# Performance work log

Hardware: AMD Instinct MI355X
Metric: run time of the kernel (lower is better)

## Reference

```python
import jax, jax.numpy as jnp
import numpy as np

B, T, H = 8, 512, 1024
NA, NP = 1024, 512
NW, WD = 16, 20          # num_width_embeddings, span_width_embedding_dim
NCLS = 66
K_ARG, K_PRED = 30, 15   # constant_arg / constant_pred caps
NEG = -1e20


def _gather_seq(seq, idx):
    # seq [B,T,D], idx [B,...] int -> [B,...,D]
    b = seq.shape[0]
    flat = idx.reshape(b, -1)
    out = jnp.take_along_axis(seq, flat[..., None], axis=1)
    return out.reshape(idx.shape + (seq.shape[-1],))


def _endpoint(features, spans, mask, W_width=None):
    mi = mask.astype(spans.dtype)
    starts = spans[..., 0] * mi
    ends = spans[..., 1] * mi
    parts = [_gather_seq(features, starts), _gather_seq(features, ends)]
    if W_width is not None:
        widths = jnp.clip(ends - starts, 0, NW - 1)
        parts.append(W_width[widths])
    return jnp.concatenate(parts, -1) * mask[..., None]


def _attentive(features, spans, mask, W_att, b_att):
    # global attention logits over all tokens [B,T]
    logits = (features @ W_att + b_att)[..., 0]
    starts, ends = spans[..., 0], spans[..., 1]
    widths = ends - starts                              # [B,N]
    r = jnp.arange(NW)                                  # static max span width
    span_mask = (r[None, None, :] <= widths[..., None])
    raw = ends[..., None] - r[None, None, :]            # AllenNLP indexes end backwards
    span_mask = span_mask & (raw >= 0)
    idx = jnp.maximum(raw, 0)                           # [B,N,W]
    emb = _gather_seq(features, idx)                    # [B,N,W,H]
    att = _gather_seq(logits[..., None], idx)[..., 0]   # [B,N,W]
    att = jnp.where(span_mask, att, -1e30)
    w = jax.nn.softmax(att, axis=-1) * span_mask
    attended = jnp.einsum('bnw,bnwh->bnh', w, emb)
    return attended * mask[..., None]


def _prune(emb, mask, num_keep, K, W1, b1, W2, b2):
    h = jax.nn.relu(emb @ W1 + b1)
    scores = h @ W2 + b2                                # [B,N,1]
    scores = jnp.where(mask[..., None] > 0, scores, NEG)
    _, top_idx = jax.lax.top_k(scores[..., 0], K)       # [B,K]
    keep = jnp.arange(K)[None, :] < num_keep[:, None]
    fill = jnp.max(top_idx, axis=1, keepdims=True)
    top_idx = jnp.where(keep, top_idx, fill)
    top_idx = jnp.sort(top_idx, axis=1)
    top_emb = jnp.take_along_axis(emb, top_idx[..., None], axis=1)
    seq_mask = jnp.take_along_axis(mask, top_idx, axis=1) > 0
    top_mask = (keep & seq_mask).astype(jnp.float32)
    top_scores = jnp.take_along_axis(scores, top_idx[..., None], axis=1)
    return top_emb, top_mask, top_idx, top_scores, scores


def setup_inputs() -> dict:
    key = jax.random.key(0)
    ks = jax.random.split(key, 16)
    features = jax.random.normal(ks[0], (B, T, H), jnp.float32)
    a_start = jax.random.randint(ks[1], (B, NA), 1, T - NW)
    a_width = jax.random.randint(ks[2], (B, NA), 0, NW)
    arg_candidates = jnp.stack([a_start, a_start + a_width], -1)
    p_start = jax.random.randint(ks[3], (B, NP), 1, T - 3)
    p_width = jax.random.randint(ks[4], (B, NP), 0, 3)
    predicate_candidates = jnp.stack([p_start, p_start + p_width], -1)

    def lin(k, i, o):
        return jax.random.normal(k, (i, o), jnp.float32) / np.sqrt(i)

    arg_dim = 3 * H + WD
    pred_dim = 2 * H
    return dict(
        features=features,
        arg_candidates=arg_candidates,
        predicate_candidates=predicate_candidates,
        W_width=jax.random.normal(ks[5], (NW, WD), jnp.float32) * 0.02,
        W_att=lin(ks[6], H, 1), b_att=jnp.zeros((1,), jnp.float32),
        Wa1=lin(ks[7], arg_dim, H), ba1=jnp.zeros((H,), jnp.float32),
        Wa2=lin(ks[8], H, 1), ba2=jnp.zeros((1,), jnp.float32),
        Wp1=lin(ks[9], pred_dim, H), bp1=jnp.zeros((H,), jnp.float32),
        Wp2=lin(ks[10], H, 1), bp2=jnp.zeros((1,), jnp.float32),
        Ws1=lin(ks[11], arg_dim + pred_dim, H), bs1=jnp.zeros((H,), jnp.float32),
        Ws2=lin(ks[12], H, NCLS - 1), bs2=jnp.zeros((NCLS - 1,), jnp.float32),
    )


def reference(features, arg_candidates, predicate_candidates, W_width, W_att, b_att,
              Wa1, ba1, Wa2, ba2, Wp1, bp1, Wp2, bp2, Ws1, bs1, Ws2, bs2):
    arg_mask = (arg_candidates[..., 1] > 0).astype(jnp.float32)
    pred_mask = (predicate_candidates[..., 1] > 0).astype(jnp.float32)

    # KENTON_LEE arg repr: endpoint (start,end,width-emb) + self-attentive
    ep = _endpoint(features, arg_candidates, arg_mask, W_width)
    at = _attentive(features, arg_candidates, arg_mask, W_att, b_att)
    arg_emb = jnp.concatenate([ep, at], -1)             # [B,NA,3H+WD]

    n_keep_arg = jnp.minimum((arg_mask.sum(-1) * 0.8).astype(jnp.int32), K_ARG)
    (top_arg_emb, top_arg_mask, top_arg_idx,
     top_arg_scores, arg_full_scores) = _prune(arg_emb, arg_mask, n_keep_arg, K_ARG, Wa1, ba1, Wa2, ba2)

    # KENTON_LEE pred repr: endpoints only (2H)
    pred_emb = _endpoint(features, predicate_candidates, pred_mask, None)
    n_keep_pred = jnp.minimum((pred_mask.sum(-1) * 0.4).astype(jnp.int32), K_PRED)
    (top_pred_emb, top_pred_mask, top_pred_idx,
     top_pred_scores, pred_full_scores) = _prune(pred_emb, pred_mask, n_keep_pred, K_PRED, Wp1, bp1, Wp2, bp2)

    top_arg_spans = jnp.take_along_axis(arg_candidates, top_arg_idx[..., None], axis=1)
    top_pred_spans = jnp.take_along_axis(predicate_candidates, top_pred_idx[..., None], axis=1)

    # pairwise scorer: concat([pred, arg]) @ Ws1 == pred@Ws1[:Dp] + arg@Ws1[Dp:]
    dp = top_pred_emb.shape[-1]
    pred_proj = top_pred_emb @ Ws1[:dp]                 # [B,Kp,H]
    arg_proj = top_arg_emb @ Ws1[dp:]                   # [B,Ka,H]
    h = jax.nn.relu(pred_proj[:, :, None, :] + arg_proj[:, None, :, :] + bs1)
    scores = h @ Ws2 + bs2                              # [B,Kp,Ka,NCLS-1]
    scores = scores + top_arg_scores[:, None, :, :] + top_pred_scores[:, :, None, :]
    dummy = jnp.zeros(scores.shape[:-1] + (1,), scores.dtype)
    srl_scores = jnp.concatenate([dummy, scores], -1)   # [B,Kp,Ka,NCLS]

    return (srl_scores, top_pred_spans, top_arg_spans, top_pred_mask,
            top_arg_mask, pred_full_scores, arg_full_scores)
```

## Files before the change

### kernel.cpp

```cpp
#include <hip/hip_runtime.h>
#include <math.h>

#define BB 8
#define TT 512
#define HH 1024
#define NAc 1024
#define NPc 512
#define NWc 16
#define WDc 20
#define NCLSc 66
#define KARG 30
#define KPRED 15
#define NEGV (-1e20f)

typedef __bf16 bf16x8 __attribute__((ext_vector_type(8)));
typedef float  f32x4  __attribute__((ext_vector_type(4)));

#define OFF_PAS   0
#define OFF_PAE   (OFF_PAS  + BB*TT*HH)
#define OFF_PATT  (OFF_PAE  + BB*TT*HH)
#define OFF_PPS   (OFF_PATT + BB*TT*HH)
#define OFF_PPE   (OFF_PPS  + BB*TT*HH)
#define OFF_END_A (OFF_PPE  + BB*TT*HH)
#define OFF_AEMB  OFF_PAS
#define OFF_PEMB  OFF_PAE
#define OFF_CPA   OFF_PATT
#define OFF_CPP   OFF_PPS
#define OFF_APROJ OFF_PPE
#define OFF_PPROJ (OFF_PPE + BB*KARG*HH)
#define OFF_LOG   OFF_END_A
#define OFF_WT    (OFF_LOG  + BB*TT)
#define OFF_AIDX  (OFF_WT   + NWc*HH)
#define OFF_PIDX  (OFF_AIDX + BB*KARG)
#define OFF_ASC   (OFF_PIDX + BB*KPRED)
#define OFF_PSC   (OFF_ASC  + BB*KARG)
#define OFF_SPLIT (OFF_PSC + BB*KPRED)
#define XSLAB_U   (4096*1024)
#define WSLAB_U   (5*1024*1024)

#define O_SRL 0
#define O_TPS (O_SRL + BB*KPRED*KARG*NCLSc)
#define O_TAS (O_TPS + BB*KPRED*2)
#define O_TPM (O_TAS + BB*KARG*2)
#define O_TAM (O_TPM + BB*KPRED)
#define O_PFS (O_TAM + BB*KARG)
#define O_AFS (O_PFS + BB*NPc)

__device__ inline float4 f4_add(const float4&a,const float4&b){return make_float4(a.x+b.x,a.y+b.y,a.z+b.z,a.w+b.w);}
__device__ inline float4 f4_fma(float c,const float4&v,const float4&a){return make_float4(fmaf(c,v.x,a.x),fmaf(c,v.y,a.y),fmaf(c,v.z,a.z),fmaf(c,v.w,a.w));}
__device__ inline float4 f4_scale(const float4&v,float c){return make_float4(v.x*c,v.y*c,v.z*c,v.w*c);}
__device__ inline float4 f4_relu(const float4&v){return make_float4(fmaxf(v.x,0.f),fmaxf(v.y,0.f),fmaxf(v.z,0.f),fmaxf(v.w,0.f));}

__device__ inline unsigned short bf16r(float f) {
  unsigned int u = __float_as_uint(f);
  u = (u + 0x7FFFu + ((u >> 16) & 1u)) >> 16;
  return (unsigned short)u;
}
__device__ inline float bf2f(unsigned short h) { return __uint_as_float(((unsigned int)h) << 16); }

__device__ inline f32x4 mfma16(bf16x8 a, bf16x8 b, f32x4 c) {
  return __builtin_amdgcn_mfma_f32_16x16x32_bf16(a, b, c, 0, 0, 0);
}

__global__ __launch_bounds__(256) void k_logits(const float* __restrict__ f, const float* __restrict__ Watt,
    const float* __restrict__ batt, float* __restrict__ lg) {
  const int lane = threadIdx.x & 63, wv = threadIdx.x >> 6;
  const int r = blockIdx.x*4 + wv;
  const float4* x = (const float4*)&f[(size_t)r*HH];
  const float4* wt = (const float4*)Watt;
  float s = 0.f;
  #pragma unroll
  for (int i=0;i<4;++i) {
    const float4 v = x[lane + i*64];
    const float4 w = wt[lane + i*64];
    s += v.x*w.x + v.y*w.y + v.z*w.z + v.w*w.w;
  }
  for (int o=32;o>0;o>>=1) s += __shfl_down(s,o,64);
  if (lane==0) lg[r] = s + batt[0];
}

__global__ __launch_bounds__(256) void k_wtab(const float* __restrict__ Wwidth, const float* __restrict__ src,
    float* __restrict__ WT) {
  const int w = blockIdx.x; const int j = threadIdx.x*4;
  float4 acc = make_float4(0,0,0,0);
  for (int d=0; d<WDc; ++d) {
    const float c = Wwidth[w*WDc+d];
    const float4 v = *(const float4*)&src[d*HH + j];
    acc = f4_fma(c, v, acc);
  }
  *(float4*)&WT[w*HH + j] = acc;
}

__global__ __launch_bounds__(256) void k_splitX(const float* __restrict__ f,
    unsigned short* __restrict__ X0, unsigned short* __restrict__ X1, unsigned short* __restrict__ X2) {
  const size_t i = ((size_t)blockIdx.x*256 + threadIdx.x) * 4;
  const float4 v = *(const float4*)&f[i];
  ushort4 h0, h1, h2;
  float a[4] = {v.x, v.y, v.z, v.w};
  unsigned short r0[4], r1[4], r2[4];
  #pragma unroll
  for (int q=0;q<4;++q) {
    r0[q] = bf16r(a[q]);            float rem1 = a[q] - bf2f(r0[q]);
    r1[q] = bf16r(rem1);            float rem2 = rem1 - bf2f(r1[q]);
    r2[q] = bf16r(rem2);
  }
  h0 = make_ushort4(r0[0],r0[1],r0[2],r0[3]);
  h1 = make_ushort4(r1[0],r1[1],r1[2],r1[3]);
  h2 = make_ushort4(r2[0],r2[1],r2[2],r2[3]);
  *(ushort4*)&X0[i] = h0;
  *(ushort4*)&X1[i] = h1;
  *(ushort4*)&X2[i] = h2;
}

__global__ __launch_bounds__(256) void k_splitW(const float* __restrict__ Wa1, const float* __restrict__ Wp1,
    unsigned short* __restrict__ W0, unsigned short* __restrict__ W1, unsigned short* __restrict__ W2) {
  const int part = blockIdx.z;
  const float* srcs[5] = {Wa1, Wa1 + 1024*1024, Wa1 + 2068*1024, Wp1, Wp1 + 1024*1024};
  const float* __restrict__ src = srcs[part];
  const size_t po = (size_t)part * 1024 * 1024;
  const int k0 = blockIdx.x * 32, n0 = blockIdx.y * 32;
  __shared__ float tile[32][33];
  const int c = threadIdx.x & 31, r0 = threadIdx.x >> 5;
  #pragma unroll
  for (int q=0;q<4;++q) {
    const int row = r0 + 8*q;
    tile[row][c] = src[(size_t)(k0+row)*1024 + n0 + c];
  }
  __syncthreads();
  #pragma unroll
  for (int q=0;q<4;++q) {
    const int nl = r0 + 8*q;
    const float v = tile[c][nl];
    const unsigned short h0 = bf16r(v);   const float rem1 = v - bf2f(h0);
    const unsigned short h1 = bf16r(rem1); const float rem2 = rem1 - bf2f(h1);
    const unsigned short h2 = bf16r(rem2);
    const size_t oi = po + (size_t)(n0+nl)*1024 + k0 + c;
    W0[oi] = h0; W1[oi] = h1; W2[oi] = h2;
  }
}

__global__ __launch_bounds__(256) void k_mgemm(
    const unsigned short* __restrict__ X0, const unsigned short* __restrict__ X1, const unsigned short* __restrict__ X2,
    const unsigned short* __restrict__ W0, const unsigned short* __restrict__ W1, const unsigned short* __restrict__ W2,
    float* __restrict__ proj) {
  const int part = blockIdx.z;
  const int rb = blockIdx.x * 128, cb = blockIdx.y * 128;
  float* __restrict__ C = proj + (size_t)part * (4096*1024);
  const size_t po = (size_t)part * 1024 * 1024;
  const unsigned short* Xs[3] = {X0, X1, X2};
  const unsigned short* Bs_[3] = {W0 + po, W1 + po, W2 + po};

  __shared__ unsigned short As[3][128*40];
  __shared__ unsigned short Bs[3][128*40];

  const int tid = threadIdx.x;
  const int lane = tid & 63, wave = tid >> 6;
  const int wr = wave >> 1, wc = wave & 1;
  const int r16 = lane & 15, g8 = (lane >> 4) * 8;

  f32x4 acc[4][4];
  #pragma unroll
  for (int i=0;i<4;++i)
    #pragma unroll
    for (int j=0;j<4;++j) acc[i][j] = (f32x4){0.f,0.f,0.f,0.f};

  for (int k0 = 0; k0 < 1024; k0 += 32) {
    for (int i = tid; i < 1536; i += 256) {
      const int slab = i >> 9, rem = i & 511, seg = rem & 3, row = rem >> 2;
      const unsigned short* src = Xs[slab] + (size_t)(rb + row) * 1024 + k0 + seg * 8;
      *(uint4*)&As[slab][row*40 + seg*8] = *(const uint4*)src;
    }
    for (int i = tid; i < 1536; i += 256) {
      const int slab = i >> 9, rem = i & 511, seg = rem & 3, row = rem >> 2;
      const unsigned short* src = Bs_[slab] + (size_t)(cb + row) * 1024 + k0 + seg * 8;
      *(uint4*)&Bs[slab][row*40 + seg*8] = *(const uint4*)src;
    }
    __syncthreads();

    bf16x8 a[3][4];
    #pragma unroll
    for (int mf=0; mf<4; ++mf) {
      const int rowi = (wr*64 + mf*16 + r16) * 40 + g8;
      a[0][mf] = *reinterpret_cast<const bf16x8*>(&As[0][rowi]);
      a[1][mf] = *reinterpret_cast<const bf16x8*>(&As[1][rowi]);
      a[2][mf] = *reinterpret_cast<const bf16x8*>(&As[2][rowi]);
    }
    #pragma unroll
    for (int nf=0; nf<4; ++nf) {
      const int rowi = (wc*64 + nf*16 + r16) * 40 + g8;
      const bf16x8 b0 = *reinterpret_cast<const bf16x8*>(&Bs[0][rowi]);
      const bf16x8 b1 = *reinterpret_cast<const bf16x8*>(&Bs[1][rowi]);
      const bf16x8 b2 = *reinterpret_cast<const bf16x8*>(&Bs[2][rowi]);
      #pragma unroll
      for (int mf=0; mf<4; ++mf) {
        f32x4 t = acc[mf][nf];
        t = mfma16(a[0][mf], b0, t);
        t = mfma16(a[0][mf], b1, t);
        t = mfma16(a[1][mf], b0, t);
        t = mfma16(a[1][mf], b1, t);
        t = mfma16(a[0][mf], b2, t);
        t = mfma16(a[2][mf], b0, t);
        acc[mf][nf] = t;
      }
    }
    __syncthreads();
  }

  const int colb = cb + wc*64 + r16;
  const int rowb = rb + wr*64 + (lane >> 4) * 4;
  #pragma unroll
  for (int mf=0; mf<4; ++mf)
    #pragma unroll
    for (int nf=0; nf<4; ++nf)
      #pragma unroll
      for (int r=0; r<4; ++r)
        C[(size_t)(rowb + mf*16 + r) * 1024 + colb + nf*16] = acc[mf][nf][r];
}

__device__ inline void att_weights(const float* __restrict__ logits, int b, int sr, int er,
                                   float aw[16], int idxs[16]) {
  const int wdt = er - sr;
  float mx = -1e30f;
  #pragma unroll
  for (int w=0; w<16; ++w) {
    const bool valid = (w <= wdt) && (er - w >= 0);
    idxs[w] = max(er - w, 0);
    aw[w] = valid ? logits[b*TT + idxs[w]] : -1e30f;
    mx = fmaxf(mx, aw[w]);
  }
  float ssum = 0.f;
  #pragma unroll
  for (int w=0; w<16; ++w) { aw[w] = expf(aw[w]-mx); ssum += aw[w]; }
  const float inv = 1.f/ssum;
  #pragma unroll
  for (int w=0; w<16; ++w) {
    const bool valid = (w <= wdt) && (er - w >= 0);
    aw[w] = valid ? aw[w]*inv : 0.f;
  }
}

__global__ __launch_bounds__(256) void k_argscore(const int* __restrict__ cand,
    const float* __restrict__ logits, const float* __restrict__ Pas, const float* __restrict__ Pae,
    const float* __restrict__ Patt, const float* __restrict__ WT,
    const float* __restrict__ ba1, const float* __restrict__ Wa2, const float* __restrict__ ba2,
    float* __restrict__ osc) {
  const int g = blockIdx.x;
  const int b = g >> 10;
  const int t = threadIdx.x;
  const int sr = cand[g*2], er = cand[g*2+1];
  if (er <= 0) { if (t==0) osc[g] = NEGV; return; }
  const int s = sr, e = er;
  const int wc = min(max(e - s, 0), NWc-1);
  float aw[16]; int idxs[16];
  att_weights(logits, b, sr, er, aw, idxs);
  float4 h = ((const float4*)&Pas[(size_t)(b*TT+s)*HH])[t];
  h = f4_add(h, ((const float4*)&Pae[(size_t)(b*TT+e)*HH])[t]);
  h = f4_add(h, ((const float4*)&WT[(size_t)wc*HH])[t]);
  #pragma unroll
  for (int w=0; w<16; ++w) if (aw[w] != 0.f) {
    const float4 v = ((const float4*)&Patt[(size_t)(b*TT+idxs[w])*HH])[t];
    h = f4_fma(aw[w], v, h);
  }
  h = f4_add(h, ((const float4*)ba1)[t]);
  h = f4_relu(h);
  const float4 w2 = ((const float4*)Wa2)[t];
  float part = h.x*w2.x + h.y*w2.y + h.z*w2.z + h.w*w2.w;
  for (int o=32;o>0;o>>=1) part += __shfl_down(part,o,64);
  __shared__ float red[4];
  const int lane = t & 63, wvi = t >> 6;
  if (lane==0) red[wvi] = part;
  __syncthreads();
  if (t==0) osc[g] = red[0]+red[1]+red[2]+red[3] + ba2[0];
}

__global__ __launch_bounds__(256) void k_predscore(const int* __restrict__ cand,
    const float* __restrict__ Pps, const float* __restrict__ Ppe,
    const float* __restrict__ bp1, const float* __restrict__ Wp2, const float* __restrict__ bp2,
    float* __restrict__ osc) {
  const int g = blockIdx.x;
  const int b = g >> 9;
  const int t = threadIdx.x;
  const int sr = cand[g*2], er = cand[g*2+1];
  if (er <= 0) { if (t==0) osc[g] = NEGV; return; }
  float4 h = ((const float4*)&Pps[(size_t)(b*TT+sr)*HH])[t];
  h = f4_add(h, ((const float4*)&Ppe[(size_t)(b*TT+er)*HH])[t]);
  h = f4_add(h, ((const float4*)bp1)[t]);
  h = f4_relu(h);
  const float4 w2 = ((const float4*)Wp2)[t];
  float part = h.x*w2.x + h.y*w2.y + h.z*w2.z + h.w*w2.w;
  for (int o=32;o>0;o>>=1) part += __shfl_down(part,o,64);
  __shared__ float red[4];
  const int lane = t & 63, wvi = t >> 6;
  if (lane==0) red[wvi] = part;
  __syncthreads();
  if (t==0) osc[g] = red[0]+red[1]+red[2]+red[3] + bp2[0];
}

__global__ __launch_bounds__(256) void k_topk(const float* __restrict__ fullsc, const int* __restrict__ cand,
    int N, int K, float frac, float* __restrict__ o_spans, float* __restrict__ o_mask,
    float* __restrict__ o_tsc, int* __restrict__ o_idx) {
  const int b = blockIdx.x;
  const int t = threadIdx.x;
  __shared__ float sv[1024];
  __shared__ int sel[32];
  __shared__ float bv[4]; __shared__ int bi[4];
  __shared__ int mcnt; __shared__ int snk;
  const float* sc = fullsc + (size_t)b*N;
  const int* cd = cand + (size_t)b*N*2;
  if (t==0) mcnt = 0;
  __syncthreads();
  int cnt = 0;
  for (int i=t;i<N;i+=256){ sv[i]=sc[i]; if (cd[i*2+1] > 0) cnt++; }
  atomicAdd(&mcnt, cnt);
  __syncthreads();
  const int lane = t & 63, wvi = t >> 6;
  for (int k=0;k<K;++k) {
    float best = -INFINITY; int bidx = 1<<30;
    for (int i=t;i<N;i+=256){ const float v=sv[i]; if (v>best){best=v;bidx=i;} }
    for (int o=32;o>0;o>>=1){
      const float v2 = __shfl_down(best,o,64); const int i2 = __shfl_down(bidx,o,64);
      if (v2>best || (v2==best && i2<bidx)) {best=v2;bidx=i2;}
    }
    if (lane==0){bv[wvi]=best;bi[wvi]=bidx;}
    __syncthreads();
    if (t==0){
      float bb=bv[0]; int ii=bi[0];
      for (int w=1;w<4;++w){ if (bv[w]>bb || (bv[w]==bb && bi[w]<ii)){bb=bv[w];ii=bi[w];} }
      sel[k]=ii; sv[ii] = -INFINITY;
    }
    __syncthreads();
  }
  if (t==0) {
    int nk = (int)((float)mcnt * frac); if (nk > K) nk = K;
    snk = nk;
    int fill = 0;
    for (int k=0;k<K;++k) fill = max(fill, sel[k]);
    for (int k=nk;k<K;++k) sel[k] = fill;
    for (int k=1;k<K;++k){ int v=sel[k]; int j=k-1; while(j>=0 && sel[j]>v){sel[j+1]=sel[j];--j;} sel[j+1]=v; }
  }
  __syncthreads();
  if (t < K) {
    const int id = sel[t];
    const int s0 = cd[id*2], e0 = cd[id*2+1];
    o_spans[(b*K+t)*2]   = (float)s0;
    o_spans[(b*K+t)*2+1] = (float)e0;
    o_mask[b*K+t] = (t < snk && e0 > 0) ? 1.f : 0.f;
    o_tsc[b*K+t] = sc[id];
    o_idx[b*K+t] = id;
  }
}

__global__ __launch_bounds__(256) void k_build_pemb(const float* __restrict__ f, const int* __restrict__ cand,
    const int* __restrict__ tidx, float* __restrict__ Pemb) {
  const int r = blockIdx.x;
  const int b = r / KPRED;
  const int id = tidx[r];
  int s = cand[(b*NPc+id)*2], e = cand[(b*NPc+id)*2+1];
  const float mf = (e > 0) ? 1.f : 0.f;
  if (e <= 0) { s = 0; e = 0; }
  const int t = threadIdx.x;
  const float4 fs = ((const float4*)&f[(size_t)(b*TT+s)*HH])[t];
  const float4 fe = ((const float4*)&f[(size_t)(b*TT+e)*HH])[t];
  float4* o = (float4*)&Pemb[(size_t)r*2048];
  o[t]     = f4_scale(fs, mf);
  o[256+t] = f4_scale(fe, mf);
}

__global__ __launch_bounds__(256) void k_build_aemb(const float* __restrict__ f, const int* __restrict__ cand,
    const int* __restrict__ tidx, const float* __restrict__ logits, const float* __restrict__ Wwidth,
    float* __restrict__ Aemb) {
  const int r = blockIdx.x;
  const int b = r / KARG;
  const int id = tidx[r];
  const int sr = cand[(b*NAc+id)*2], er = cand[(b*NAc+id)*2+1];
  const float mf = (er > 0) ? 1.f : 0.f;
  const int s = (er > 0) ? sr : 0, e = (er > 0) ? er : 0;
  const int wc = min(max(e - s, 0), NWc-1);
  float aw[16]; int idxs[16];
  att_weights(logits, b, sr, er, aw, idxs);
  const int t = threadIdx.x;
  float* rowp = &Aemb[(size_t)r*3092];
  const float4 fs  = ((const float4*)&f[(size_t)(b*TT+s)*HH])[t];
  const float4 fe4 = ((const float4*)&f[(size_t)(b*TT+e)*HH])[t];
  ((float4*)rowp)[t]        = f4_scale(fs, mf);
  ((float4*)(rowp+1024))[t] = f4_scale(fe4, mf);
  if (t < WDc) rowp[2048+t] = Wwidth[wc*WDc+t]*mf;
  float4 acc = make_float4(0,0,0,0);
  #pragma unroll
  for (int w=0; w<16; ++w) if (aw[w] != 0.f) {
    const float4 fv = ((const float4*)&f[(size_t)(b*TT+idxs[w])*HH])[t];
    acc = f4_fma(aw[w], fv, acc);
  }
  ((float4*)(rowp+2068))[t] = f4_scale(acc, mf);
}

template<int MT>
__global__ __launch_bounds__(256) void k_sgemm(const float* __restrict__ A, int lda, int K,
                                               const float* __restrict__ W, float* __restrict__ Cp) {
  const int ct = blockIdx.x;
  const int b  = blockIdx.y;
  const int kz = blockIdx.z;
  const int Mtotal = 8*MT;
  const int cbase = ct*128;
  const int rbase = b*MT;
  const int klen = K/4;
  const int kbeg = kz*klen, kend = kbeg + klen;
  __shared__ float As[MT][64];
  const int tid = threadIdx.x;
  const int lane = tid & 63, wv = tid >> 6;
  const int ks = lane & 7;
  const int cg = wv*8 + (lane >> 3);
  const int col = cbase + cg*4;
  float acc[MT][4];
  #pragma unroll
  for (int m=0;m<MT;++m){acc[m][0]=0.f;acc[m][1]=0.f;acc[m][2]=0.f;acc[m][3]=0.f;}
  for (int k0 = kbeg; k0 < kend; k0 += 64) {
    const int kc = min(64, kend - k0);
    for (int i = tid; i < MT*64; i += 256) {
      const int m = i >> 6, kk = i & 63;
      As[m][kk] = (kk < kc) ? A[(size_t)(rbase+m)*lda + k0 + kk] : 0.f;
    }
    __syncthreads();
    const int kmax = min(8, kc - ks*8);
    for (int i = 0; i < kmax; ++i) {
      const int kk = ks*8 + i;
      const float4 wv4 = *(const float4*)&W[(size_t)(k0+kk)*1024 + col];
      #pragma unroll
      for (int m=0;m<MT;++m) {
        const float av = As[m][kk];
        acc[m][0] = fmaf(av, wv4.x, acc[m][0]);
        acc[m][1] = fmaf(av, wv4.y, acc[m][1]);
        acc[m][2] = fmaf(av, wv4.z, acc[m][2]);
        acc[m][3] = fmaf(av, wv4.w, acc[m][3]);
      }
    }
    __syncthreads();
  }
  #pragma unroll
  for (int m=0;m<MT;++m) {
    #pragma unroll
    for (int j=0;j<4;++j) {
      float v = acc[m][j];
      v += __shfl_xor(v, 1, 64);
      v += __shfl_xor(v, 2, 64);
      v += __shfl_xor(v, 4, 64);
      acc[m][j] = v;
    }
  }
  if (ks == 0) {
    #pragma unroll
    for (int m=0;m<MT;++m) {
      const float4 v = make_float4(acc[m][0],acc[m][1],acc[m][2],acc[m][3]);
      *(float4*)&Cp[((size_t)kz*Mtotal + rbase + m)*1024 + col] = v;
    }
  }
}

__global__ void k_reduce4(const float* __restrict__ Cp, float* __restrict__ Co, int n) {
  const int i = blockIdx.x*256 + threadIdx.x;
  if (i < n) Co[i] = Cp[i] + Cp[(size_t)n+i] + Cp[2*(size_t)n+i] + Cp[3*(size_t)n+i];
}

__global__ __launch_bounds__(256) void k_final(const float* __restrict__ pproj, const float* __restrict__ aproj,
    const float* __restrict__ bs1, const float* __restrict__ Ws2, const float* __restrict__ bs2,
    const float* __restrict__ tasc, const float* __restrict__ tpsc, float* __restrict__ srl) {
  const int g = blockIdx.x;
  const int b = g / (KPRED*KARG);
  const int rem = g % (KPRED*KARG);
  const int p = rem / KARG, a = rem % KARG;
  const int t = threadIdx.x;
  __shared__ float h[1024];
  __shared__ float part[4][64];
  __shared__ float r64[4];
  {
    const float4 pv = ((const float4*)&pproj[(size_t)(b*KPRED+p)*HH])[t];
    const float4 av = ((const float4*)&aproj[(size_t)(b*KARG+a)*HH])[t];
    const float4 bv = ((const float4*)bs1)[t];
    float4 v;
    v.x = fmaxf(pv.x+av.x+bv.x, 0.f);
    v.y = fmaxf(pv.y+av.y+bv.y, 0.f);
    v.z = fmaxf(pv.z+av.z+bv.z, 0.f);
    v.w = fmaxf(pv.w+av.w+bv.w, 0.f);
    ((float4*)h)[t] = v;
  }
  __syncthreads();
  const int j = t & 63, sl = t >> 6;
  float accj = 0.f, acc64 = 0.f;
  const int kb = sl*256;
  for (int kk = kb; kk < kb+256; ++kk) {
    const float hv = h[kk];
    accj = fmaf(hv, Ws2[(size_t)kk*65 + j], accj);
    if (j == 0) acc64 = fmaf(hv, Ws2[(size_t)kk*65 + 64], acc64);
  }
  part[sl][j] = accj;
  if (j == 0) r64[sl] = acc64;
  __syncthreads();
  const float base = tasc[b*KARG+a] + tpsc[b*KPRED+p];
  float* o = &srl[(size_t)g*NCLSc];
  if (t < 64) {
    o[1+t] = part[0][t]+part[1][t]+part[2][t]+part[3][t] + bs2[t] + base;
  } else if (t == 64) {
    o[0] = 0.f;
    o[65] = r64[0]+r64[1]+r64[2]+r64[3] + bs2[64] + base;
  }
}

extern "C" void kernel_launch(void* const* d_in, const int* in_sizes, int n_in,
                              void* d_out, int out_size, void* d_ws, size_t ws_size,
                              hipStream_t stream) {
  const float* features = (const float*)d_in[0];
  const int*   argc_    = (const int*)d_in[1];
  const int*   predc    = (const int*)d_in[2];
  const float* Wwidth   = (const float*)d_in[3];
  const float* Watt     = (const float*)d_in[4];
  const float* batt     = (const float*)d_in[5];
  const float* Wa1      = (const float*)d_in[6];
  const float* ba1      = (const float*)d_in[7];
  const float* Wa2      = (const float*)d_in[8];
  const float* ba2      = (const float*)d_in[9];
  const float* Wp1      = (const float*)d_in[10];
  const float* bp1      = (const float*)d_in[11];
  const float* Wp2      = (const float*)d_in[12];
  const float* bp2      = (const float*)d_in[13];
  const float* Ws1      = (const float*)d_in[14];
  const float* bs1      = (const float*)d_in[15];
  const float* Ws2      = (const float*)d_in[16];
  const float* bs2      = (const float*)d_in[17];
  float* ws  = (float*)d_ws;
  float* out = (float*)d_out;

  unsigned short* X0 = (unsigned short*)(ws + OFF_SPLIT);
  unsigned short* X1 = X0 + XSLAB_U;
  unsigned short* X2 = X1 + XSLAB_U;
  unsigned short* W0 = X2 + XSLAB_U;
  unsigned short* W1 = W0 + WSLAB_U;
  unsigned short* W2 = W1 + WSLAB_U;

  k_logits<<<dim3(BB*TT/4), 256, 0, stream>>>(features, Watt, batt, ws + OFF_LOG);
  k_wtab<<<dim3(NWc), 256, 0, stream>>>(Wwidth, Wa1 + 2048*1024, ws + OFF_WT);
  k_splitX<<<dim3(4096), 256, 0, stream>>>(features, X0, X1, X2);
  k_splitW<<<dim3(32, 32, 5), 256, 0, stream>>>(Wa1, Wp1, W0, W1, W2);
  k_mgemm<<<dim3(32, 8, 5), 256, 0, stream>>>(X0, X1, X2, W0, W1, W2, ws + OFF_PAS);
  k_argscore<<<dim3(BB*NAc), 256, 0, stream>>>(argc_, ws + OFF_LOG, ws + OFF_PAS, ws + OFF_PAE,
      ws + OFF_PATT, ws + OFF_WT, ba1, Wa2, ba2, out + O_AFS);
  k_predscore<<<dim3(BB*NPc), 256, 0, stream>>>(predc, ws + OFF_PPS, ws + OFF_PPE,
      bp1, Wp2, bp2, out + O_PFS);
  k_topk<<<dim3(BB), 256, 0, stream>>>(out + O_AFS, argc_, NAc, KARG, 0.8f,
      out + O_TAS, out + O_TAM, ws + OFF_ASC, (int*)(ws + OFF_AIDX));
  k_topk<<<dim3(BB), 256, 0, stream>>>(out + O_PFS, predc, NPc, KPRED, 0.4f,
      out + O_TPS, out + O_TPM, ws + OFF_PSC, (int*)(ws + OFF_PIDX));
  k_build_aemb<<<dim3(BB*KARG), 256, 0, stream>>>(features, argc_, (const int*)(ws + OFF_AIDX),
      ws + OFF_LOG, Wwidth, ws + OFF_AEMB);
  k_build_pemb<<<dim3(BB*KPRED), 256, 0, stream>>>(features, predc, (const int*)(ws + OFF_PIDX),
      ws + OFF_PEMB);
  k_sgemm<KARG><<<dim3(8, 8, 4), 256, 0, stream>>>(ws + OFF_AEMB, 3092, 3092, Ws1 + (size_t)2048*1024, ws + OFF_CPA);
  k_sgemm<KPRED><<<dim3(8, 8, 4), 256, 0, stream>>>(ws + OFF_PEMB, 2048, 2048, Ws1, ws + OFF_CPP);
  k_reduce4<<<dim3((BB*KARG*HH + 255)/256), 256, 0, stream>>>(ws + OFF_CPA, ws + OFF_APROJ, BB*KARG*HH);
  k_reduce4<<<dim3((BB*KPRED*HH + 255)/256), 256, 0, stream>>>(ws + OFF_CPP, ws + OFF_PPROJ, BB*KPRED*HH);
  k_final<<<dim3(BB*KPRED*KARG), 256, 0, stream>>>(ws + OFF_PPROJ, ws + OFF_APROJ,
      bs1, Ws2, bs2, ws + OFF_ASC, ws + OFF_PSC, out + O_SRL);
}
```

Baseline: 955.2 us.

## Restructure split-bf16 GEMM into six passes with direct global-to-LDS loads

The three-way split-bf16 GEMM no longer stages all three slabs of A and B in shared memory per k-step. It now runs six sequential passes over the term pairs (X0W0, X0W1, X1W0, X1W1, X0W2, X2W0), each loading a 128x64 tile straight into LDS with global_load_lds. This cuts LDS footprint and register pressure and removes the VGPR round-trip on loads, which may raise occupancy. The cost is that each A/B slab is re-read from global memory several times, and the unpadded 64-wide LDS rows may cause bank conflicts on the fragment reads.

```diff
diff --git a/kernel.cpp b/kernel.cpp
--- a/kernel.cpp
+++ b/kernel.cpp
@@ -15,6 +15,9 @@
 
 typedef __bf16 bf16x8 __attribute__((ext_vector_type(8)));
 typedef float  f32x4  __attribute__((ext_vector_type(4)));
+
+#define LDS_U32(p) ((__attribute__((address_space(3))) unsigned int*)(p))
+#define GLB_U32(p) ((const __attribute__((address_space(1))) unsigned int*)(p))
 
 #define OFF_PAS   0
 #define OFF_PAE   (OFF_PAS  + BB*TT*HH)
@@ -95,7 +98,6 @@
     unsigned short* __restrict__ X0, unsigned short* __restrict__ X1, unsigned short* __restrict__ X2) {
   const size_t i = ((size_t)blockIdx.x*256 + threadIdx.x) * 4;
   const float4 v = *(const float4*)&f[i];
-  ushort4 h0, h1, h2;
   float a[4] = {v.x, v.y, v.z, v.w};
   unsigned short r0[4], r1[4], r2[4];
   #pragma unroll
@@ -104,12 +106,9 @@
     r1[q] = bf16r(rem1);            float rem2 = rem1 - bf2f(r1[q]);
     r2[q] = bf16r(rem2);
   }
-  h0 = make_ushort4(r0[0],r0[1],r0[2],r0[3]);
-  h1 = make_ushort4(r1[0],r1[1],r1[2],r1[3]);
-  h2 = make_ushort4(r2[0],r2[1],r2[2],r2[3]);
-  *(ushort4*)&X0[i] = h0;
-  *(ushort4*)&X1[i] = h1;
-  *(ushort4*)&X2[i] = h2;
+  *(ushort4*)&X0[i] = make_ushort4(r0[0],r0[1],r0[2],r0[3]);
+  *(ushort4*)&X1[i] = make_ushort4(r1[0],r1[1],r1[2],r1[3]);
+  *(ushort4*)&X2[i] = make_ushort4(r2[0],r2[1],r2[2],r2[3]);
 }
 
 __global__ __launch_bounds__(256) void k_splitW(const float* __restrict__ Wa1, const float* __restrict__ Wp1,
@@ -147,63 +146,62 @@
   const int rb = blockIdx.x * 128, cb = blockIdx.y * 128;
   float* __restrict__ C = proj + (size_t)part * (4096*1024);
   const size_t po = (size_t)part * 1024 * 1024;
-  const unsigned short* Xs[3] = {X0, X1, X2};
-  const unsigned short* Bs_[3] = {W0 + po, W1 + po, W2 + po};
-
-  __shared__ unsigned short As[3][128*40];
-  __shared__ unsigned short Bs[3][128*40];
+
+  __shared__ unsigned short As[128][64];
+  __shared__ unsigned short Bs[128][64];
 
   const int tid = threadIdx.x;
   const int lane = tid & 63, wave = tid >> 6;
   const int wr = wave >> 1, wc = wave & 1;
   const int r16 = lane & 15, g8 = (lane >> 4) * 8;
 
+  const int srow = (lane >> 3);
+  const int sseg = (lane & 7) * 8;
+
   f32x4 acc[4][4];
   #pragma unroll
   for (int i=0;i<4;++i)
     #pragma unroll
     for (int j=0;j<4;++j) acc[i][j] = (f32x4){0.f,0.f,0.f,0.f};
 
-  for (int k0 = 0; k0 < 1024; k0 += 32) {
-    for (int i = tid; i < 1536; i += 256) {
-      const int slab = i >> 9, rem = i & 511, seg = rem & 3, row = rem >> 2;
-      const unsigned short* src = Xs[slab] + (size_t)(rb + row) * 1024 + k0 + seg * 8;
-      *(uint4*)&As[slab][row*40 + seg*8] = *(const uint4*)src;
-    }
-    for (int i = tid; i < 1536; i += 256) {
-      const int slab = i >> 9, rem = i & 511, seg = rem & 3, row = rem >> 2;
-      const unsigned short* src = Bs_[slab] + (size_t)(cb + row) * 1024 + k0 + seg * 8;
-      *(uint4*)&Bs[slab][row*40 + seg*8] = *(const uint4*)src;
-    }
-    __syncthreads();
-
-    bf16x8 a[3][4];
-    #pragma unroll
-    for (int mf=0; mf<4; ++mf) {
-      const int rowi = (wr*64 + mf*16 + r16) * 40 + g8;
-      a[0][mf] = *reinterpret_cast<const bf16x8*>(&As[0][rowi]);
-      a[1][mf] = *reinterpret_cast<const bf16x8*>(&As[1][rowi]);
-      a[2][mf] = *reinterpret_cast<const bf16x8*>(&As[2][rowi]);
-    }
-    #pragma unroll
-    for (int nf=0; nf<4; ++nf) {
-      const int rowi = (wc*64 + nf*16 + r16) * 40 + g8;
-      const bf16x8 b0 = *reinterpret_cast<const bf16x8*>(&Bs[0][rowi]);
-      const bf16x8 b1 = *reinterpret_cast<const bf16x8*>(&Bs[1][rowi]);
-      const bf16x8 b2 = *reinterpret_cast<const bf16x8*>(&Bs[2][rowi]);
+  const unsigned short* const XA[6] = {X0, X0, X1, X1, X0, X2};
+  const unsigned short* const WB[6] = {W0+po, W1+po, W0+po, W1+po, W2+po, W0+po};
+
+  #pragma unroll
+  for (int t = 0; t < 6; ++t) {
+    const unsigned short* __restrict__ ap = XA[t];
+    const unsigned short* __restrict__ bp = WB[t];
+    for (int kc = 0; kc < 16; ++kc) {
+      const int kbase = kc * 64;
       #pragma unroll
-      for (int mf=0; mf<4; ++mf) {
-        f32x4 t = acc[mf][nf];
-        t = mfma16(a[0][mf], b0, t);
-        t = mfma16(a[0][mf], b1, t);
-        t = mfma16(a[1][mf], b0, t);
-        t = mfma16(a[1][mf], b1, t);
-        t = mfma16(a[0][mf], b2, t);
-        t = mfma16(a[2][mf], b0, t);
-        acc[mf][nf] = t;
+      for (int i = 0; i < 4; ++i) {
+        const int rl = wave*32 + i*8;
+        __builtin_amdgcn_global_load_lds(
+            GLB_U32(ap + (size_t)(rb + rl + srow)*1024 + kbase + sseg),
+            LDS_U32(&As[rl][0]), 16, 0, 0);
+        __builtin_amdgcn_global_load_lds(
+            GLB_U32(bp + (size_t)(cb + rl + srow)*1024 + kbase + sseg),
+            LDS_U32(&Bs[rl][0]), 16, 0, 0);
       }
-    }
-    __syncthreads();
+      __syncthreads();
+
+      #pragma unroll
+      for (int ks = 0; ks < 2; ++ks) {
+        bf16x8 a[4], b[4];
+        #pragma unroll
+        for (int mf=0; mf<4; ++mf)
+          a[mf] = *reinterpret_cast<const bf16x8*>(&As[wr*64 + mf*16 + r16][ks*32 + g8]);
+        #pragma unroll
+        for (int nf=0; nf<4; ++nf)
+          b[nf] = *reinterpret_cast<const bf16x8*>(&Bs[wc*64 + nf*16 + r16][ks*32 + g8]);
+        #pragma unroll
+        for (int mf=0; mf<4; ++mf)
+          #pragma unroll
+          for (int nf=0; nf<4; ++nf)
+            acc[mf][nf] = mfma16(a[mf], b[nf], acc[mf][nf]);
+      }
+      __syncthreads();
+    }
   }
 
   const int colb = cb + wc*64 + r16;
```

New measurement: 964.4 us. Within noise of the previous version (+1.0%).
